# Optimization experiments

Measured on AMD Instinct MI355X. Metric: run time of the kernel, lower is better.

## Reference

```python
import jax, jax.numpy as jnp
import numpy as np

DT = 0.01
REG = 0.01

def setup_inputs() -> dict:
    key = jax.random.key(0)
    k1, k2, k3, k4 = jax.random.split(key, 4)
    B, C_in, L = 16, 128, 4096
    C_out, KS = 256, 9
    return {
        "x": jax.random.normal(k1, (B, C_in, L), dtype=jnp.float32),
        "weight": jax.random.normal(k2, (C_out, C_in, KS), dtype=jnp.float32) * np.sqrt(2.0 / (C_out * KS)),
        "bias": jnp.zeros((C_out,), dtype=jnp.float32),
        "vel": jax.random.normal(k3, (C_in, KS), dtype=jnp.float32) * 0.1,
        "acc": jax.random.normal(k4, (C_in, KS), dtype=jnp.float32) * 0.01,
        "ks": 9,
        "stride": 1,
        "pad": 4,
    }

def reference(x, weight, bias, vel, acc, ks, stride, pad):
    # x: [B, C_in, L]
    if pad > 0:
        x = jnp.pad(x, ((0, 0), (0, 0), (pad, pad)), mode="edge")  # replicate pad
    L_pad = x.shape[2]
    L_out = (L_pad - ks) // stride + 1
    t_off = jnp.arange(ks, dtype=jnp.float32) * DT  # [ks]
    # unfold: gather sliding windows -> [B, C_in, L_out, ks]
    idx = jnp.arange(L_out)[:, None] * stride + jnp.arange(ks)[None, :]
    xu = x[:, :, idx]
    # per-tap physics offset: vel*t + 0.5*acc*t^2, shape [C_in, ks] broadcast
    offset = vel * t_off + 0.5 * acc * (t_off ** 2)  # [C_in, ks]
    xt = xu + offset[None, :, None, :]  # [B, C_in, L_out, ks]
    # GEMM: [B, L_out, C_in*ks] x [C_in*ks, C_out]
    out = jnp.einsum("bclk,ock->bol", xt, weight) + bias[None, :, None]
    phys = REG * (jnp.mean(vel ** 2) + jnp.mean(acc ** 2))
    return (out, phys)
```

## Files before the change

### kernel.cpp

```cpp
#include <hip/hip_runtime.h>
#include <hip/hip_bf16.h>

typedef unsigned short u16;
typedef __bf16 bf16x8 __attribute__((ext_vector_type(8)));
typedef float f32x4 __attribute__((ext_vector_type(4)));
typedef float f32x16 __attribute__((ext_vector_type(16)));
typedef unsigned short ushort8 __attribute__((ext_vector_type(8)));

#define C_IN   128
#define C_OUT  256
#define BATCH  16
#define LEN    4096
#define KS     9
#define PAD    4
#define KTOT   (C_IN * KS)
#define NSTEP  72

#define W5_BLKS    1152
#define EB_BLKS    256

__device__ inline u16 f2bf(float f) {
    __hip_bfloat16 h = __float2bfloat16(f);
    return __builtin_bit_cast(u16, h);
}

__device__ __forceinline__ void g2l16(const void* g, void* l) {
    __builtin_amdgcn_global_load_lds(
        (const __attribute__((address_space(1))) void*)g,
        (__attribute__((address_space(3))) void*)l, 16, 0, 0);
}

__global__ void prep_all(const float* __restrict__ w,
                         const float* __restrict__ bias, const float* __restrict__ vel,
                         const float* __restrict__ acc_in,
                         u16* __restrict__ w5,
                         float* __restrict__ ebias, float* __restrict__ phys_out) {
    int bid = blockIdx.x;
    int t = threadIdx.x;
    if (bid < W5_BLKS) {
        int i = bid * 256 + t;
        int e    = i & 7;
        int lane = (i >> 3) & 63;
        int g    = (i >> 9) & 7;
        int s    = i >> 12;
        int o    = g * 32 + (lane & 31);
        int hi   = lane >> 5;
        int c    = (s & 7) * 16 + hi * 8 + e;
        int k    = s >> 3;
        w5[i] = f2bf(w[((size_t)o * C_IN + c) * KS + k]);
        return;
    }
    __shared__ float red[256];
    int o = bid - W5_BLKS;
    float sum = 0.f;
    for (int i = t; i < KTOT; i += 256) {
        int k = i % KS;
        float tk = k * 0.01f;
        float off = vel[i] * tk + 0.5f * acc_in[i] * tk * tk;
        sum += off * w[(size_t)o * KTOT + i];
    }
    red[t] = sum;
    __syncthreads();
    for (int h = 128; h > 0; h >>= 1) {
        if (t < h) red[t] += red[t + h];
        __syncthreads();
    }
    if (t == 0) ebias[o] = bias[o] + red[0];

    if (o == 0) {
        __syncthreads();
        float pv = 0.f;
        for (int i = t; i < KTOT; i += 256) {
            float v = vel[i], a = acc_in[i];
            pv += v * v + a * a;
        }
        red[t] = pv;
        __syncthreads();
        for (int h = 128; h > 0; h >>= 1) {
            if (t < h) red[t] += red[t + h];
            __syncthreads();
        }
        if (t == 0) *phys_out = 0.01f * (red[0] / (float)KTOT);
    }
}

__global__ __launch_bounds__(128, 1) void conv_main(const float* __restrict__ x,
                                                    const u16* __restrict__ w5,
                                                    const float* __restrict__ ebias,
                                                    float* __restrict__ out) {
    __shared__ u16 ldsx[17408];

    int b     = blockIdx.y;
    int lbase = blockIdx.x * 128;
    int t     = threadIdx.x;
    int lane  = t & 63;
    int wm    = t >> 6;
    int l31   = lane & 31;
    int hi    = lane >> 5;

    const u16* alane = w5 + ((size_t)(wm * 4) * 64 + lane) * 8;

    #define LOAD_A(S, AF)                                                        \
        {                                                                        \
            const u16* p_ = alane + (size_t)(S) * 4096;                          \
            _Pragma("unroll")                                                    \
            for (int mi = 0; mi < 4; ++mi)                                       \
                AF[mi] = *reinterpret_cast<const bf16x8*>(p_ + mi * 512);        \
        }
    #define LOAD_B(S, BF)                                                        \
        {                                                                        \
            int k_ = (S) >> 3;                                                   \
            int sl_ = ((S) & 7) * 2 + hi;                                        \
            _Pragma("unroll")                                                    \
            for (int nj = 0; nj < 4; ++nj) {                                     \
                int row_  = nj * 32 + l31 + k_;                                  \
                int addr_ = row_ * 256 + ((sl_ ^ (row_ & 15)) << 4);             \
                BF[nj] = *reinterpret_cast<const bf16x8*>(ldsbase + addr_);      \
            }                                                                    \
        }
    #define MFMA16(AF, BF)                                                       \
        {                                                                        \
            _Pragma("unroll")                                                    \
            for (int mi = 0; mi < 4; ++mi)                                       \
                _Pragma("unroll")                                                \
                for (int nj = 0; nj < 4; ++nj)                                   \
                    acc[mi][nj] = __builtin_amdgcn_mfma_f32_32x32x16_bf16(       \
                        AF[mi], BF[nj], acc[mi][nj], 0, 0, 0);                   \
        }

    bf16x8 aA[4], aB[4], bA[4], bB[4];
    LOAD_A(0, aA);

    const float* xb = x + (size_t)b * C_IN * LEN;
    {
        int r = t;
        int l = lbase + r - PAD;
        l = l < 0 ? 0 : (l > LEN - 1 ? LEN - 1 : l);
        int key = r & 15;
        float v[16][8];
        #pragma unroll
        for (int cb = 0; cb < 16; ++cb)
            #pragma unroll
            for (int e = 0; e < 8; ++e)
                v[cb][e] = xb[(size_t)(cb * 8 + e) * LEN + l];
        #pragma unroll
        for (int cb = 0; cb < 16; ++cb) {
            ushort8 u;
            #pragma unroll
            for (int e = 0; e < 8; ++e) u[e] = f2bf(v[cb][e]);
            *reinterpret_cast<ushort8*>(ldsx + r * 128 + ((cb ^ key) * 8)) = u;
        }
    }
    {
        int r  = 128 + (t & 7);
        int cb = t >> 3;
        int l = lbase + r - PAD;
        l = l < 0 ? 0 : (l > LEN - 1 ? LEN - 1 : l);
        ushort8 u;
        #pragma unroll
        for (int e = 0; e < 8; ++e)
            u[e] = f2bf(xb[(size_t)(cb * 8 + e) * LEN + l]);
        *reinterpret_cast<ushort8*>(ldsx + r * 128 + ((cb ^ (r & 15)) * 8)) = u;
    }
    __syncthreads();

    f32x16 acc[4][4] = {};
    const char* ldsbase = reinterpret_cast<const char*>(ldsx);
    LOAD_B(0, bA);

    #pragma unroll
    for (int s = 0; s < NSTEP; s += 2) {
        LOAD_A(s + 1, aB);
        LOAD_B(s + 1, bB);
        MFMA16(aA, bA);
        if (s + 2 < NSTEP) { LOAD_A(s + 2, aA); LOAD_B(s + 2, bA); }
        MFMA16(aB, bB);
    }

    #pragma unroll
    for (int mi = 0; mi < 4; ++mi) {
        int o0 = wm * 128 + mi * 32 + hi * 4;
        #pragma unroll
        for (int nj = 0; nj < 4; ++nj) {
            int l = lbase + nj * 32 + l31;
            #pragma unroll
            for (int q = 0; q < 4; ++q) {
                f32x4 eb = *reinterpret_cast<const f32x4*>(ebias + o0 + q * 8);
                float* op = out + (size_t)(b * C_OUT + o0 + q * 8) * LEN + l;
                #pragma unroll
                for (int p = 0; p < 4; ++p)
                    op[(size_t)p * LEN] = acc[mi][nj][q * 4 + p] + eb[p];
            }
        }
    }
    #undef LOAD_A
    #undef LOAD_B
    #undef MFMA16
}

extern "C" void kernel_launch(void* const* d_in, const int* in_sizes, int n_in,
                              void* d_out, int out_size, void* d_ws, size_t ws_size,
                              hipStream_t stream) {
    const float* x      = (const float*)d_in[0];
    const float* weight = (const float*)d_in[1];
    const float* bias   = (const float*)d_in[2];
    const float* vel    = (const float*)d_in[3];
    const float* acc    = (const float*)d_in[4];
    float* out = (float*)d_out;

    char* ws = (char*)d_ws;
    u16*  w5    = (u16*)ws;
    float* ebias = (float*)(ws + (size_t)C_OUT * KTOT * 2);

    hipLaunchKernelGGL(prep_all, dim3(W5_BLKS + EB_BLKS), dim3(256), 0, stream,
                       weight, bias, vel, acc, w5, ebias,
                       out + (size_t)BATCH * C_OUT * LEN);
    hipLaunchKernelGGL(conv_main, dim3(LEN / 128, BATCH), dim3(128), 0, stream,
                       x, w5, ebias, out);
}
```

Baseline: 51.79 us.

## Stage weights through LDS ring buffer with 4-wave blocks splitting N

Each block now runs four waves in a 2x2 split instead of two waves. Previously each wave read its own weight fragments straight from global memory; now the weight slices are staged into LDS through a 4-slot ring using global_load_lds, prefetched three steps ahead and shared by the waves. Explicit waitcnt and barriers synchronise every step, and setprio raises priority around the MFMA section. Per-wave accumulator registers are halved, allowing two blocks per CU, but the per-step barriers and the extra LDS traffic may cost throughput.

```diff
diff --git a/kernel.cpp b/kernel.cpp
--- a/kernel.cpp
+++ b/kernel.cpp
@@ -84,105 +84,118 @@
     }
 }
 
-__global__ __launch_bounds__(128, 1) void conv_main(const float* __restrict__ x,
+__global__ __launch_bounds__(256, 2) void conv_main(const float* __restrict__ x,
                                                     const u16* __restrict__ w5,
                                                     const float* __restrict__ ebias,
                                                     float* __restrict__ out) {
     __shared__ u16 ldsx[17408];
+    __shared__ u16 ldsa[4][4096];
 
     int b     = blockIdx.y;
     int lbase = blockIdx.x * 128;
     int t     = threadIdx.x;
     int lane  = t & 63;
-    int wm    = t >> 6;
+    int w     = t >> 6;
+    int wm    = w >> 1;
+    int wn    = w & 1;
     int l31   = lane & 31;
     int hi    = lane >> 5;
 
-    const u16* alane = w5 + ((size_t)(wm * 4) * 64 + lane) * 8;
-
-    #define LOAD_A(S, AF)                                                        \
-        {                                                                        \
-            const u16* p_ = alane + (size_t)(S) * 4096;                          \
+    #define LOAD_A(SLOT, AF)                                                     \
+        {                                                                        \
+            const u16* ab_ = ldsa[SLOT] + (wm * 4) * 512 + lane * 8;             \
             _Pragma("unroll")                                                    \
             for (int mi = 0; mi < 4; ++mi)                                       \
-                AF[mi] = *reinterpret_cast<const bf16x8*>(p_ + mi * 512);        \
+                AF[mi] = *reinterpret_cast<const bf16x8*>(ab_ + mi * 512);       \
         }
     #define LOAD_B(S, BF)                                                        \
         {                                                                        \
             int k_ = (S) >> 3;                                                   \
             int sl_ = ((S) & 7) * 2 + hi;                                        \
             _Pragma("unroll")                                                    \
-            for (int nj = 0; nj < 4; ++nj) {                                     \
-                int row_  = nj * 32 + l31 + k_;                                  \
+            for (int nj = 0; nj < 2; ++nj) {                                     \
+                int row_  = wn * 64 + nj * 32 + l31 + k_;                        \
                 int addr_ = row_ * 256 + ((sl_ ^ (row_ & 15)) << 4);             \
                 BF[nj] = *reinterpret_cast<const bf16x8*>(ldsbase + addr_);      \
             }                                                                    \
         }
-    #define MFMA16(AF, BF)                                                       \
+    #define STAGE_A(S)                                                           \
+        {                                                                        \
+            const u16* as_ = w5 + (size_t)(S) * 4096;                            \
+            u16* ad_ = ldsa[(S) & 3];                                            \
+            _Pragma("unroll")                                                    \
+            for (int j = 0; j < 2; ++j)                                          \
+                g2l16(as_ + (j * 256 + t) * 8, ad_ + (j * 256 + w * 64) * 8);    \
+        }
+    #define MFMA8(AF, BF)                                                        \
         {                                                                        \
             _Pragma("unroll")                                                    \
             for (int mi = 0; mi < 4; ++mi)                                       \
                 _Pragma("unroll")                                                \
-                for (int nj = 0; nj < 4; ++nj)                                   \
+                for (int nj = 0; nj < 2; ++nj)                                   \
                     acc[mi][nj] = __builtin_amdgcn_mfma_f32_32x32x16_bf16(       \
                         AF[mi], BF[nj], acc[mi][nj], 0, 0, 0);                   \
         }
 
-    bf16x8 aA[4], aB[4], bA[4], bB[4];
-    LOAD_A(0, aA);
-
     const float* xb = x + (size_t)b * C_IN * LEN;
     {
-        int r = t;
-        int l = lbase + r - PAD;
-        l = l < 0 ? 0 : (l > LEN - 1 ? LEN - 1 : l);
-        int key = r & 15;
-        float v[16][8];
-        #pragma unroll
-        for (int cb = 0; cb < 16; ++cb)
+        STAGE_A(0); STAGE_A(1); STAGE_A(2);
+        if (t < 128) {
+            int r = t;
+            int l = lbase + r - PAD;
+            l = l < 0 ? 0 : (l > LEN - 1 ? LEN - 1 : l);
+            int key = r & 15;
+            #pragma unroll
+            for (int cb = 0; cb < 16; ++cb) {
+                ushort8 u;
+                #pragma unroll
+                for (int e = 0; e < 8; ++e)
+                    u[e] = f2bf(xb[(size_t)(cb * 8 + e) * LEN + l]);
+                *reinterpret_cast<ushort8*>(ldsx + r * 128 + ((cb ^ key) * 8)) = u;
+            }
+        } else {
+            int u2 = t - 128;
+            int r  = 128 + (u2 >> 4);
+            int cb = u2 & 15;
+            int l = lbase + r - PAD;
+            l = l < 0 ? 0 : (l > LEN - 1 ? LEN - 1 : l);
+            ushort8 u;
             #pragma unroll
             for (int e = 0; e < 8; ++e)
-                v[cb][e] = xb[(size_t)(cb * 8 + e) * LEN + l];
-        #pragma unroll
-        for (int cb = 0; cb < 16; ++cb) {
-            ushort8 u;
-            #pragma unroll
-            for (int e = 0; e < 8; ++e) u[e] = f2bf(v[cb][e]);
-            *reinterpret_cast<ushort8*>(ldsx + r * 128 + ((cb ^ key) * 8)) = u;
-        }
-    }
-    {
-        int r  = 128 + (t & 7);
-        int cb = t >> 3;
-        int l = lbase + r - PAD;
-        l = l < 0 ? 0 : (l > LEN - 1 ? LEN - 1 : l);
-        ushort8 u;
-        #pragma unroll
-        for (int e = 0; e < 8; ++e)
-            u[e] = f2bf(xb[(size_t)(cb * 8 + e) * LEN + l]);
-        *reinterpret_cast<ushort8*>(ldsx + r * 128 + ((cb ^ (r & 15)) * 8)) = u;
-    }
-    __syncthreads();
-
-    f32x16 acc[4][4] = {};
+                u[e] = f2bf(xb[(size_t)(cb * 8 + e) * LEN + l]);
+            *reinterpret_cast<ushort8*>(ldsx + r * 128 + ((cb ^ (r & 15)) * 8)) = u;
+        }
+    }
+    asm volatile("s_waitcnt vmcnt(4) lgkmcnt(0)" ::: "memory");
+    __builtin_amdgcn_s_barrier();
+
+    f32x16 acc[4][2] = {};
     const char* ldsbase = reinterpret_cast<const char*>(ldsx);
-    LOAD_B(0, bA);
 
     #pragma unroll
-    for (int s = 0; s < NSTEP; s += 2) {
-        LOAD_A(s + 1, aB);
-        LOAD_B(s + 1, bB);
-        MFMA16(aA, bA);
-        if (s + 2 < NSTEP) { LOAD_A(s + 2, aA); LOAD_B(s + 2, bA); }
-        MFMA16(aB, bB);
+    for (int s = 0; s < NSTEP; ++s) {
+        bf16x8 af[4], bf[2];
+        LOAD_A(s & 3, af);
+        LOAD_B(s, bf);
+        if (s + 3 < NSTEP) STAGE_A(s + 3);
+        if (s + 3 < NSTEP)      asm volatile("s_waitcnt vmcnt(4)" ::: "memory");
+        else if (s + 2 < NSTEP) asm volatile("s_waitcnt vmcnt(2)" ::: "memory");
+        else                    asm volatile("s_waitcnt vmcnt(0)" ::: "memory");
+        __builtin_amdgcn_s_barrier();
+        asm volatile("s_waitcnt lgkmcnt(0)" ::: "memory");
+        __builtin_amdgcn_sched_barrier(0);
+        __builtin_amdgcn_s_setprio(1);
+        MFMA8(af, bf);
+        __builtin_amdgcn_s_setprio(0);
+        if (s + 1 < NSTEP) __builtin_amdgcn_s_barrier();
     }
 
     #pragma unroll
     for (int mi = 0; mi < 4; ++mi) {
         int o0 = wm * 128 + mi * 32 + hi * 4;
         #pragma unroll
-        for (int nj = 0; nj < 4; ++nj) {
-            int l = lbase + nj * 32 + l31;
+        for (int nj = 0; nj < 2; ++nj) {
+            int l = lbase + wn * 64 + nj * 32 + l31;
             #pragma unroll
             for (int q = 0; q < 4; ++q) {
                 f32x4 eb = *reinterpret_cast<const f32x4*>(ebias + o0 + q * 8);
@@ -195,7 +208,8 @@
     }
     #undef LOAD_A
     #undef LOAD_B
-    #undef MFMA16
+    #undef STAGE_A
+    #undef MFMA8
 }
 
 extern "C" void kernel_launch(void* const* d_in, const int* in_sizes, int n_in,
@@ -215,6 +229,6 @@
     hipLaunchKernelGGL(prep_all, dim3(W5_BLKS + EB_BLKS), dim3(256), 0, stream,
                        weight, bias, vel, acc, w5, ebias,
                        out + (size_t)BATCH * C_OUT * LEN);
-    hipLaunchKernelGGL(conv_main, dim3(LEN / 128, BATCH), dim3(128), 0, stream,
+    hipLaunchKernelGGL(conv_main, dim3(LEN / 128, BATCH), dim3(256), 0, stream,
                        x, w5, ebias, out);
 }
```

New measurement: 54.04 us. 1.04x slower.
